# Optimization experiments

Hardware: AMD Instinct MI355X
Metric: run time of the kernel (lower is better)

## Reference

```python
import jax, jax.numpy as jnp
import numpy as np

B, S, HID, H, D, F = 8, 256, 1024, 16, 64, 64
BASE_LR = 0.1
MAX_STEPS = 4
EPS = 1e-5


def _ln(x, g, b):
    mu = jnp.mean(x, axis=-1, keepdims=True)
    var = jnp.var(x, axis=-1, keepdims=True)
    return (x - mu) * jax.lax.rsqrt(var + EPS) * g + b


def setup_inputs() -> dict:
    key = jax.random.key(0)
    ks = jax.random.split(key, 10)
    n = lambda i, shape, s=0.02: jax.random.normal(ks[i], shape, jnp.float32) * s
    return {
        "x": jax.random.normal(ks[0], (B, S, HID), jnp.float32),
        "wq": n(1, (HID, HID)),
        "wk": n(2, (HID, HID)),
        "wv": n(3, (HID, HID)),
        "fw_w1": n(4, (H, D, F), 0.05),
        "fw_b1": jnp.zeros((H, F), jnp.float32),
        "fw_w2": n(5, (H, F, D), 0.05),
        "fw_b2": jnp.zeros((H, D), jnp.float32),
        "fw_ln_g": jnp.ones((H, D), jnp.float32),
        "fw_ln_b": jnp.zeros((H, D), jnp.float32),
        "loss_w": n(6, (D, D)),
        "loss_b": jnp.zeros((D,), jnp.float32),
        "ttt_g": jnp.ones((H, D), jnp.float32),
        "ttt_b": jnp.zeros((H, D), jnp.float32),
        "wo": n(7, (HID, HID)),
        "wg": n(8, (HID, HID)),
        "pn_g": jnp.ones((HID,), jnp.float32),
        "pn_b": jnp.zeros((HID,), jnp.float32),
    }


def _fw_apply(p, kx):
    # per-head fast-weight MLP: kx (B,H,D) -> (B,H,D)
    w1, b1, w2, b2, lg, lb = p
    h = jax.nn.gelu(jnp.einsum('bhd,hdf->bhf', kx, w1) + b1)
    o = jnp.einsum('bhf,hfd->bhd', h, w2) + b2
    return _ln(o, lg, lb)


def _forward(x, wq, wk, wv, fw_w1, fw_b1, fw_w2, fw_b2, fw_ln_g, fw_ln_b,
             loss_w, loss_b, ttt_g, ttt_b, wo, wg, pn_g, pn_b):
    # projections (torch Linear with W stored as (in,out) here: y = x @ W)
    q = (x @ wq).reshape(B, S, H, D)
    k = (x @ wk).reshape(B, S, H, D)
    v = (x @ wv).reshape(B, S, H, D)
    # scan over tokens: xs shaped (S, B, H, D)
    qs = jnp.swapaxes(q, 0, 1)
    ks_ = jnp.swapaxes(k, 0, 1)
    vs = jnp.swapaxes(v, 0, 1)

    def token_step(p, qkv):
        q_t, k_t, v_t = qkv  # (B,H,D) each
        target = v_t - k_t

        def loss_fn(pp):
            z = _fw_apply(pp, k_t)
            pred = jnp.einsum('bhd,de->bhe', z, loss_w) + loss_b
            return jnp.mean((pred - target) ** 2)

        for _ in range(MAX_STEPS):
            g = jax.grad(loss_fn)(p)
            p = jax.tree.map(lambda a, gg: a - BASE_LR * gg, p, g)
        z = _fw_apply(p, k_t)
        z = _ln(z, ttt_g, ttt_b)  # per-head post-TTT LayerNorm
        return p, q_t + z

    p0 = (fw_w1, fw_b1, fw_w2, fw_b2, fw_ln_g, fw_ln_b)
    _, outs = jax.lax.scan(token_step, p0, (qs, ks_, vs))
    out = jnp.swapaxes(outs, 0, 1).reshape(B, S, HID)
    gated = jax.nn.gelu(x @ wg) * _ln(out, pn_g, pn_b)
    return gated @ wo


def reference(x, wq, wk, wv, fw_w1, fw_b1, fw_w2, fw_b2, fw_ln_g, fw_ln_b,
              loss_w, loss_b, ttt_g, ttt_b, wo, wg, pn_g, pn_b):
    return _forward(x, wq, wk, wv, fw_w1, fw_b1, fw_w2, fw_b2, fw_ln_g, fw_ln_b,
                    loss_w, loss_b, ttt_g, ttt_b, wo, wg, pn_g, pn_b)
```

## Files before the change

### kernel.cpp

```cpp
#include <hip/hip_runtime.h>

#define Bv 8
#define Sv 256
#define Hv 16
#define Dv 64
#define LR 0.1f
#define SCALE (2.0f / 8192.0f)

using bf16x8 = __attribute__((ext_vector_type(8))) short;
using bf16x4 = __attribute__((ext_vector_type(4))) short;
using f32x4  = __attribute__((ext_vector_type(4))) float;
using u32x4  = __attribute__((ext_vector_type(4))) unsigned;
#define MFMA16(A, B, C) __builtin_amdgcn_mfma_f32_16x16x32_bf16(A, B, C, 0, 0, 0)

constexpr int U_W1T = 0;
constexpr int U_W2T = 8704;
constexpr int U_W2R = 17408;
constexpr int U_G   = 26112;
constexpr int U_LwR = 34816;
constexpr int U_K   = 43520;
constexpr int U_H   = 45696;
constexpr int U_Z   = 47872;
constexpr int U_TG  = 50048;
constexpr int U_DO  = 52224;
constexpr int U_KT  = 54400;
constexpr int U_HT  = 55424;
constexpr int U_DOT = 56448;
constexpr int U_DAT = 57472;
constexpr int F_BASE = 29248;
constexpr int F_O   = F_BASE;
constexpr int F_XH  = F_BASE + 544;
constexpr int F_GD  = F_XH + 544;
constexpr int F_TGL = F_GD + 544;
constexpr int F_B1  = F_TGL + 544;
constexpr int F_B2  = F_B1 + 64;
constexpr int F_LG  = F_B2 + 64;
constexpr int F_LB  = F_LG + 64;
constexpr int F_C1  = F_LB + 64;
constexpr int F_TGm = F_C1 + 64;
constexpr int F_TBm = F_TGm + 64;
constexpr int F_RSTD = F_TBm + 64;
constexpr int U_KG  = (F_RSTD + 8) * 2;
constexpr int U_HT2 = U_KG + 256;
constexpr int LDS_BYTES = (U_HT2 + 1024) * 2;

__device__ __forceinline__ short bf_rn(float v) {
    unsigned u = __float_as_uint(v);
    unsigned r = u + 0x7fffu + ((u >> 16) & 1u);
    return (short)(r >> 16);
}
__device__ __forceinline__ void cvt1(float v, short &hi, short &lo) {
    hi = bf_rn(v);
    float hf = __uint_as_float(((unsigned)(unsigned short)hi) << 16);
    lo = bf_rn(v - hf);
}
__device__ __forceinline__ float bf2f(short u) {
    return __uint_as_float(((unsigned)(unsigned short)u) << 16);
}
__device__ __forceinline__ unsigned cvtpk(float a, float b) {
    unsigned r;
    asm("v_cvt_pk_bf16_f32 %0, %1, %2" : "=v"(r) : "v"(a), "v"(b));
    return r;
}
__device__ __forceinline__ void cvt2(float a, float b, unsigned &hw,
                                     unsigned &lw) {
    hw = cvtpk(a, b);
    float ra = a - __uint_as_float(hw << 16);
    float rb = b - __uint_as_float(hw & 0xffff0000u);
    lw = cvtpk(ra, rb);
}
template <int CTRL>
__device__ __forceinline__ float dpp_add(float v) {
    int s = __builtin_amdgcn_update_dpp(0, __float_as_int(v), CTRL, 0xF, 0xF,
                                        true);
    return v + __int_as_float(s);
}
__device__ __forceinline__ float red32(float v) {
    v = dpp_add<0xB1>(v);
    v = dpp_add<0x4E>(v);
    v = dpp_add<0x124>(v);
    v = dpp_add<0x128>(v);
    v += __shfl_xor(v, 16);
    return v;
}
__device__ __forceinline__ float fast_tanh(float u) {
    u = fminf(fmaxf(u, -10.f), 10.f);
    float e = __expf(2.0f * u);
    return (e - 1.0f) / (e + 1.0f);
}
__device__ __forceinline__ void gelu_both(float x, float &g, float &dg) {
    const float C0 = 0.7978845608028654f, A0 = 0.044715f;
    float x2 = x * x;
    float u = C0 * x * (1.0f + A0 * x2);
    float t = fast_tanh(u);
    g = 0.5f * x * (1.0f + t);
    float du = C0 * (1.0f + 3.0f * A0 * x2);
    dg = 0.5f * (1.0f + t) + 0.5f * x * (1.0f - t * t) * du;
}
__device__ __forceinline__ float gelu_f(float x) {
    const float C0 = 0.7978845608028654f, A0 = 0.044715f;
    float u = C0 * x * (1.0f + A0 * x * x);
    return 0.5f * x * (1.0f + fast_tanh(u));
}

__device__ __forceinline__ f32x4 mm64(const unsigned short *Ap,
                                      const unsigned short *Bp,
                                      int w, int c, int q) {
    const unsigned short *ar = Ap + c * 136 + 8 * q;
    const unsigned short *br = Bp + (16 * w + c) * 136 + 8 * q;
    bf16x8 ah0 = *(const bf16x8 *)(ar);
    bf16x8 al0 = *(const bf16x8 *)(ar + 64);
    bf16x8 bh0 = *(const bf16x8 *)(br);
    bf16x8 bl0 = *(const bf16x8 *)(br + 64);
    bf16x8 ah1 = *(const bf16x8 *)(ar + 32);
    bf16x8 al1 = *(const bf16x8 *)(ar + 96);
    bf16x8 bh1 = *(const bf16x8 *)(br + 32);
    bf16x8 bl1 = *(const bf16x8 *)(br + 96);
    f32x4 x0 = {0.f, 0.f, 0.f, 0.f}, x1 = {0.f, 0.f, 0.f, 0.f};
    x0 = MFMA16(ah0, bh0, x0); x1 = MFMA16(ah1, bh1, x1);
    x0 = MFMA16(al0, bh0, x0); x1 = MFMA16(al1, bh1, x1);
    x0 = MFMA16(ah0, bl0, x0); x1 = MFMA16(ah1, bl1, x1);
    return x0 + x1;
}

__device__ __forceinline__ void updW3(const bf16x8 *a4, bf16x8 b,
                                      float (&m)[16], unsigned short *WT,
                                      int w, int c, int q) {
    f32x4 g[4];
#pragma unroll
    for (int mt = 0; mt < 4; ++mt) {
        f32x4 z = {0.f, 0.f, 0.f, 0.f};
        g[mt] = MFMA16(a4[mt], b, z);
    }
    unsigned short *p0 = &WT[(16 * w + c) * 136 + 4 * q];
#pragma unroll
    for (int mt = 0; mt < 4; ++mt) {
        m[mt * 4 + 0] -= LR * g[mt][0];
        m[mt * 4 + 1] -= LR * g[mt][1];
        m[mt * 4 + 2] -= LR * g[mt][2];
        m[mt * 4 + 3] -= LR * g[mt][3];
        unsigned nh0, nl0, nh1, nl1;
        cvt2(m[mt * 4 + 0], m[mt * 4 + 1], nh0, nl0);
        cvt2(m[mt * 4 + 2], m[mt * 4 + 3], nh1, nl1);
        uint2 nh, nl;
        nh.x = nh0; nh.y = nh1;
        nl.x = nl0; nl.y = nl1;
        *(uint2 *)(p0 + 16 * mt) = nh;
        *(uint2 *)(p0 + 16 * mt + 64) = nl;
    }
}

__global__ __launch_bounds__(256) void ttt_scan(
    const float *__restrict__ q_g, const float *__restrict__ k_g,
    const float *__restrict__ v_g, float *__restrict__ out_g,
    const float *__restrict__ fw_w1, const float *__restrict__ fw_b1,
    const float *__restrict__ fw_w2, const float *__restrict__ fw_b2,
    const float *__restrict__ fw_lng, const float *__restrict__ fw_lnb,
    const float *__restrict__ loss_w, const float *__restrict__ loss_bv,
    const float *__restrict__ ttt_gv, const float *__restrict__ ttt_bv) {
    extern __shared__ char smem[];
    unsigned short *us = (unsigned short *)smem;
    float *fs = (float *)smem;

    unsigned short *W1T = us + U_W1T, *W2T = us + U_W2T, *W2R = us + U_W2R;
    unsigned short *Gp = us + U_G, *LwR = us + U_LwR;
    unsigned short *Kp = us + U_K, *Hp = us + U_H, *Zp = us + U_Z;
    unsigned short *TGp = us + U_TG, *DOp = us + U_DO;
    unsigned short *KT = us + U_KT, *HT0 = us + U_HT;
    unsigned short *DOT = us + U_DOT;
    unsigned short *KgT = us + U_KG, *HT1 = us + U_HT2;
    float *o_s = fs + F_O, *xh_s = fs + F_XH;
    float *b2_s = fs + F_B2, *lg_s = fs + F_LG;
    float *lb_s = fs + F_LB, *c1_s = fs + F_C1;
    float *tG_s = fs + F_TGm, *tB_s = fs + F_TBm, *rstd_s = fs + F_RSTD;

    const int h = blockIdx.x, tid = threadIdx.x;
    const int w = tid >> 6, lane = tid & 63, c = lane & 15, q = lane >> 4;
    const int bb = tid >> 5, j0 = (tid & 31) * 2;

    for (int i = tid; i < 4096; i += 256) {
        int r = i >> 6, cc = i & 63;
        short hi, lo;
        cvt1(fw_w1[h * 4096 + i], hi, lo);
        W1T[cc * 136 + r] = (unsigned short)hi;
        W1T[cc * 136 + 64 + r] = (unsigned short)lo;
        cvt1(fw_w2[h * 4096 + i], hi, lo);
        W2T[cc * 136 + r] = (unsigned short)hi;
        W2T[cc * 136 + 64 + r] = (unsigned short)lo;
        W2R[r * 136 + cc] = (unsigned short)hi;
        W2R[r * 136 + 64 + cc] = (unsigned short)lo;
        cvt1(loss_w[i], hi, lo);
        LwR[r * 136 + cc] = (unsigned short)hi;
        LwR[r * 136 + 64 + cc] = (unsigned short)lo;
    }
    for (int i = tid; i < 5 * 8 * 128; i += 256) {
        int a = i / 128, u = i % 128;
        int arr = a >> 3, row = 8 + (a & 7);
        unsigned short *base = (arr == 0) ? Kp : (arr == 1) ? Hp
                              : (arr == 2) ? Zp : (arr == 3) ? TGp : DOp;
        base[row * 136 + u] = 0;
    }
    float w1m[16], w2m[16], w2rm[16];
#pragma unroll
    for (int mt = 0; mt < 4; ++mt) {
#pragma unroll
        for (int r = 0; r < 4; ++r) {
            int el = 16 * mt + 4 * q + r;
            int row = 16 * w + c;
            w1m[mt * 4 + r] = fw_w1[h * 4096 + el * 64 + row];
            w2m[mt * 4 + r] = fw_w2[h * 4096 + el * 64 + row];
            w2rm[mt * 4 + r] = fw_w2[h * 4096 + row * 64 + el];
        }
    }
    __syncthreads();
#pragma unroll 1
    for (int mt = 0; mt < 4; ++mt) {
        f32x4 g = mm64(LwR + 16 * 136 * mt, LwR, w, c, q);
#pragma unroll
        for (int r = 0; r < 4; ++r) {
            short hi, lo;
            cvt1(g[r], hi, lo);
            int dr = 16 * mt + 4 * q + r, dc = 16 * w + c;
            Gp[dr * 136 + dc] = (unsigned short)hi;
            Gp[dr * 136 + 64 + dc] = (unsigned short)lo;
        }
    }
    if (tid < 64) {
        b2_s[tid] = fw_b2[h * 64 + tid];
        lg_s[tid] = fw_lng[h * 64 + tid];
        lb_s[tid] = fw_lnb[h * 64 + tid];
        tG_s[tid] = ttt_gv[h * 64 + tid];
        tB_s[tid] = ttt_bv[h * 64 + tid];
        float c1 = 0.f;
        for (int e = 0; e < 64; ++e) c1 += loss_bv[e] * loss_w[tid * 64 + e];
        c1_s[tid] = c1;
    }

    float2 pk, pv, pq, q_cur;
    {
        int idx = ((bb * Sv + 0) * Hv + h) * Dv + j0;
        float2 k0 = *(const float2 *)&k_g[idx];
        float2 v0 = *(const float2 *)&v_g[idx];
        q_cur = *(const float2 *)&q_g[idx];
        unsigned khw, klw;
        cvt2(k0.x, k0.y, khw, klw);
        *(unsigned *)&Kp[bb * 136 + j0] = khw;
        *(unsigned *)&Kp[bb * 136 + 64 + j0] = klw;
        KT[j0 * 16 + bb] = (unsigned short)khw;
        KT[j0 * 16 + 8 + bb] = (unsigned short)klw;
        KT[(j0 + 1) * 16 + bb] = (unsigned short)(khw >> 16);
        KT[(j0 + 1) * 16 + 8 + bb] = (unsigned short)(klw >> 16);
        unsigned thw, tlw;
        cvt2(v0.x - k0.x, v0.y - k0.y, thw, tlw);
        *(unsigned *)&TGp[bb * 136 + j0] = thw;
        *(unsigned *)&TGp[bb * 136 + 64 + j0] = tlw;
    }
    float b1_r = (q < 2) ? fw_b1[h * 64 + 16 * w + c] : 0.f;
    __syncthreads();
    float c1_r = c1_s[16 * w + c];
    f32x4 gd_r = {0.f, 0.f, 0.f, 0.f};
    f32x4 tgl_r = {0.f, 0.f, 0.f, 0.f};

#pragma unroll 1
    for (int t = 0; t < Sv; ++t) {
        if (t + 1 < Sv) {
            int idx2 = ((bb * Sv + t + 1) * Hv + h) * Dv + j0;
            pk = *(const float2 *)&k_g[idx2];
            pv = *(const float2 *)&v_g[idx2];
            pq = *(const float2 *)&q_g[idx2];
        }

        f32x4 acc1 = mm64(Kp, W1T, w, c, q);
        {
            f32x4 a2 = mm64(TGp, LwR, w, c, q);
            if (q < 2) {
#pragma unroll
                for (int r = 0; r < 4; ++r) tgl_r[r] = a2[r] - c1_r;
            }
        }
        if (w == 0) {
            f32x4 kg = mm64(Kp, Kp, 0, c, q);
            if (q < 2) {
#pragma unroll
                for (int r = 0; r < 4; ++r) {
                    short hi, lo;
                    cvt1(-LR * kg[r], hi, lo);
                    KgT[c * 16 + 4 * q + r] = (unsigned short)hi;
                    KgT[c * 16 + 8 + 4 * q + r] = (unsigned short)lo;
                }
            }
        }
        if (q < 2) {
            int col = 16 * w + c;
            float gv[4];
#pragma unroll
            for (int r = 0; r < 4; ++r) {
                float g, dg;
                gelu_both(acc1[r] + b1_r, g, dg);
                gv[r] = g;
                gd_r[r] = dg;
            }
            unsigned h01, l01, h23, l23;
            cvt2(gv[0], gv[1], h01, l01);
            cvt2(gv[2], gv[3], h23, l23);
            Hp[(4 * q + 0) * 136 + col] = (unsigned short)h01;
            Hp[(4 * q + 1) * 136 + col] = (unsigned short)(h01 >> 16);
            Hp[(4 * q + 2) * 136 + col] = (unsigned short)h23;
            Hp[(4 * q + 3) * 136 + col] = (unsigned short)(h23 >> 16);
            Hp[(4 * q + 0) * 136 + 64 + col] = (unsigned short)l01;
            Hp[(4 * q + 1) * 136 + 64 + col] = (unsigned short)(l01 >> 16);
            Hp[(4 * q + 2) * 136 + 64 + col] = (unsigned short)l23;
            Hp[(4 * q + 3) * 136 + 64 + col] = (unsigned short)(l23 >> 16);
            uint2 hh, hl;
            hh.x = h01; hh.y = h23;
            hl.x = l01; hl.y = l23;
            *(uint2 *)&HT0[col * 16 + 4 * q] = hh;
            *(uint2 *)&HT0[col * 16 + 8 + 4 * q] = hl;
        }
        __syncthreads();

#pragma unroll 1
        for (int step = 0; step < 4; ++step) {
            const unsigned short *HTr = (step & 1) ? HT1 : HT0;
            unsigned short *HTw = (step & 1) ? HT0 : HT1;
            f32x4 acc = mm64(Hp, W2T, w, c, q);
            if (q < 2) {
                float bias = b2_s[16 * w + c];
#pragma unroll
                for (int r = 0; r < 4; ++r)
                    o_s[(4 * q + r) * 68 + 16 * w + c] = acc[r] + bias;
            }
            __syncthreads();
            float xh0_r, xh1_r;
            {
                float2 xv = *(const float2 *)&o_s[bb * 68 + j0];
                float s = red32(xv.x + xv.y);
                float s2 = red32(xv.x * xv.x + xv.y * xv.y);
                float mu = s * (1.f / 64.f);
                float var = s2 * (1.f / 64.f) - mu * mu;
                float rs = rsqrtf(var + 1e-5f);
                float xh0 = (xv.x - mu) * rs, xh1 = (xv.y - mu) * rs;
                float2 xw; xw.x = xh0; xw.y = xh1;
                *(float2 *)&xh_s[bb * 68 + j0] = xw;
                float z0 = xh0 * lg_s[j0] + lb_s[j0];
                float z1 = xh1 * lg_s[j0 + 1] + lb_s[j0 + 1];
                unsigned zh, zl;
                cvt2(z0, z1, zh, zl);
                *(unsigned *)&Zp[bb * 136 + j0] = zh;
                *(unsigned *)&Zp[bb * 136 + 64 + j0] = zl;
                if ((tid & 31) == 0) rstd_s[bb] = rs;
                xh0_r = xh0; xh1_r = xh1;
            }
            __syncthreads();
            acc = mm64(Zp, Gp, w, c, q);
            if (q < 2) {
                int col = 16 * w + c;
#pragma unroll
                for (int r = 0; r < 4; ++r)
                    o_s[(4 * q + r) * 68 + col] = (acc[r] - tgl_r[r]) * SCALE;
            }
            __syncthreads();
            {
                float2 dzv = *(const float2 *)&o_s[bb * 68 + j0];
                float dxh0 = dzv.x * lg_s[j0], dxh1 = dzv.y * lg_s[j0 + 1];
                float S1 = red32(dxh0 + dxh1) * (1.f / 64.f);
                float S2 = red32(dxh0 * xh0_r + dxh1 * xh1_r) * (1.f / 64.f);
                float rs = rstd_s[bb];
                float do0 = rs * (dxh0 - S1 - xh0_r * S2);
                float do1 = rs * (dxh1 - S1 - xh1_r * S2);
                unsigned dh, dl;
                cvt2(do0, do1, dh, dl);
                *(unsigned *)&DOp[bb * 136 + j0] = dh;
                *(unsigned *)&DOp[bb * 136 + 64 + j0] = dl;
                DOT[j0 * 16 + bb] = (unsigned short)dh;
                DOT[j0 * 16 + 8 + bb] = (unsigned short)dl;
                DOT[(j0 + 1) * 16 + bb] = (unsigned short)(dh >> 16);
                DOT[(j0 + 1) * 16 + 8 + bb] = (unsigned short)(dl >> 16);
            }
            __syncthreads();
            bf16x8 zf8;
#pragma unroll
            for (int j = 0; j < 8; ++j) zf8[j] = 0;
            bf16x8 aK[4], aH[4], aD[4];
#pragma unroll
            for (int mt = 0; mt < 4; ++mt) {
                aK[mt] = *(const bf16x8 *)&KT[(16 * mt + c) * 16 + (q & 1) * 8];
                aH[mt] = *(const bf16x8 *)&HTr[(16 * mt + c) * 16 + (q & 1) * 8];
                aD[mt] = *(const bf16x8 *)&DOT[(16 * mt + c) * 16 + (q & 1) * 8];
            }
            bf16x8 bDO = zf8, bHT = zf8;
            if (q < 2) {
                bDO = *(const bf16x8 *)&DOT[(16 * w + c) * 16];
                bHT = *(const bf16x8 *)&HTr[(16 * w + c) * 16];
            } else if (q == 2) {
                bDO = *(const bf16x8 *)&DOT[(16 * w + c) * 16 + 8];
                bHT = *(const bf16x8 *)&HTr[(16 * w + c) * 16 + 8];
            }
            bf16x8 aKg = *(const bf16x8 *)&KgT[c * 16 + (q & 1) * 8];
            acc = mm64(DOp, W2R, w, c, q);
            {
                float b1sum = 0.f;
                uint2 th; th.x = 0u; th.y = 0u;
                uint2 tl; tl.x = 0u; tl.y = 0u;
                if (q < 2) {
                    float da0 = acc[0] * gd_r[0];
                    float da1 = acc[1] * gd_r[1];
                    float da2 = acc[2] * gd_r[2];
                    float da3 = acc[3] * gd_r[3];
                    b1sum = da0 + da1 + da2 + da3;
                    unsigned h01, l01, h23, l23;
                    cvt2(da0, da1, h01, l01);
                    cvt2(da2, da3, h23, l23);
                    th.x = h01; th.y = h23;
                    tl.x = l01; tl.y = l23;
                }
                b1sum += __shfl_xor(b1sum, 16);
                unsigned hx0 = (unsigned)__shfl((int)th.x, c);
                unsigned hy0 = (unsigned)__shfl((int)th.y, c);
                unsigned hx1 = (unsigned)__shfl((int)th.x, c + 16);
                unsigned hy1 = (unsigned)__shfl((int)th.y, c + 16);
                unsigned lx0 = (unsigned)__shfl((int)tl.x, c);
                unsigned ly0 = (unsigned)__shfl((int)tl.y, c);
                unsigned lx1 = (unsigned)__shfl((int)tl.x, c + 16);
                unsigned ly1 = (unsigned)__shfl((int)tl.y, c + 16);
                u32x4 Bw = {0u, 0u, 0u, 0u};
                if (q < 2) {
                    Bw[0] = hx0; Bw[1] = hy0; Bw[2] = hx1; Bw[3] = hy1;
                } else if (q == 2) {
                    Bw[0] = lx0; Bw[1] = ly0; Bw[2] = lx1; Bw[3] = ly1;
                }
                bf16x8 bDA = __builtin_bit_cast(bf16x8, Bw);
                updW3(aK, bDA, w1m, W1T, w, c, q);
                updW3(aH, bDO, w2m, W2T, w, c, q);
                updW3(aD, bHT, w2rm, W2R, w, c, q);
                if (w == 2) {
                    bf16x8 oh_ = *(const bf16x8 *)&DOT[lane * 16];
                    bf16x8 ol_ = *(const bf16x8 *)&DOT[lane * 16 + 8];
                    float db2 = 0.f;
#pragma unroll
                    for (int j = 0; j < 8; ++j)
                        db2 += bf2f(oh_[j]) + bf2f(ol_[j]);
                    b2_s[lane] -= LR * db2;
                } else if (w == 3) {
                    float dlb = 0.f, dlg = 0.f;
#pragma unroll
                    for (int b = 0; b < 8; ++b) {
                        float dzv = o_s[b * 68 + lane];
                        dlb += dzv;
                        dlg += dzv * xh_s[b * 68 + lane];
                    }
                    lb_s[lane] -= LR * dlb;
                    lg_s[lane] -= LR * dlg;
                }
                acc1 = MFMA16(aKg, bDA, acc1);
                b1_r -= LR * b1sum;
                if (q < 2) {
                    int col = 16 * w + c;
                    if (step < 3) {
                        float gv[4];
#pragma unroll
                        for (int r = 0; r < 4; ++r) {
                            float g, dg;
                            gelu_both(acc1[r] + b1_r, g, dg);
                            gv[r] = g;
                            gd_r[r] = dg;
                        }
                        unsigned h01, l01, h23, l23;
                        cvt2(gv[0], gv[1], h01, l01);
                        cvt2(gv[2], gv[3], h23, l23);
                        Hp[(4 * q + 0) * 136 + col] = (unsigned short)h01;
                        Hp[(4 * q + 1) * 136 + col] = (unsigned short)(h01 >> 16);
                        Hp[(4 * q + 2) * 136 + col] = (unsigned short)h23;
                        Hp[(4 * q + 3) * 136 + col] = (unsigned short)(h23 >> 16);
                        Hp[(4 * q + 0) * 136 + 64 + col] = (unsigned short)l01;
                        Hp[(4 * q + 1) * 136 + 64 + col] = (unsigned short)(l01 >> 16);
                        Hp[(4 * q + 2) * 136 + 64 + col] = (unsigned short)l23;
                        Hp[(4 * q + 3) * 136 + 64 + col] = (unsigned short)(l23 >> 16);
                        uint2 hh, hl;
                        hh.x = h01; hh.y = h23;
                        hl.x = l01; hl.y = l23;
                        *(uint2 *)&HTw[col * 16 + 4 * q] = hh;
                        *(uint2 *)&HTw[col * 16 + 8 + 4 * q] = hl;
                    } else {
                        float gv[4];
#pragma unroll
                        for (int r = 0; r < 4; ++r)
                            gv[r] = gelu_f(acc1[r] + b1_r);
                        unsigned h01, l01, h23, l23;
                        cvt2(gv[0], gv[1], h01, l01);
                        cvt2(gv[2], gv[3], h23, l23);
                        Hp[(4 * q + 0) * 136 + col] = (unsigned short)h01;
                        Hp[(4 * q + 1) * 136 + col] = (unsigned short)(h01 >> 16);
                        Hp[(4 * q + 2) * 136 + col] = (unsigned short)h23;
                        Hp[(4 * q + 3) * 136 + col] = (unsigned short)(h23 >> 16);
                        Hp[(4 * q + 0) * 136 + 64 + col] = (unsigned short)l01;
                        Hp[(4 * q + 1) * 136 + 64 + col] = (unsigned short)(l01 >> 16);
                        Hp[(4 * q + 2) * 136 + 64 + col] = (unsigned short)l23;
                        Hp[(4 * q + 3) * 136 + 64 + col] = (unsigned short)(l23 >> 16);
                    }
                }
            }
            __syncthreads();
        }

        f32x4 acc = mm64(Hp, W2T, w, c, q);
        if (q < 2) {
            float bias = b2_s[16 * w + c];
#pragma unroll
            for (int r = 0; r < 4; ++r)
                o_s[(4 * q + r) * 68 + 16 * w + c] = acc[r] + bias;
        }
        if (t + 1 < Sv) {
            unsigned khw, klw;
            cvt2(pk.x, pk.y, khw, klw);
            *(unsigned *)&Kp[bb * 136 + j0] = khw;
            *(unsigned *)&Kp[bb * 136 + 64 + j0] = klw;
            KT[j0 * 16 + bb] = (unsigned short)khw;
            KT[j0 * 16 + 8 + bb] = (unsigned short)klw;
            KT[(j0 + 1) * 16 + bb] = (unsigned short)(khw >> 16);
            KT[(j0 + 1) * 16 + 8 + bb] = (unsigned short)(klw >> 16);
            unsigned thw, tlw;
            cvt2(pv.x - pk.x, pv.y - pk.y, thw, tlw);
            *(unsigned *)&TGp[bb * 136 + j0] = thw;
            *(unsigned *)&TGp[bb * 136 + 64 + j0] = tlw;
        }
        __syncthreads();
        {
            float2 xv = *(const float2 *)&o_s[bb * 68 + j0];
            float s = red32(xv.x + xv.y);
            float s2 = red32(xv.x * xv.x + xv.y * xv.y);
            float mu = s * (1.f / 64.f);
            float var = s2 * (1.f / 64.f) - mu * mu;
            float rs = rsqrtf(var + 1e-5f);
            float z0 = (xv.x - mu) * rs * lg_s[j0] + lb_s[j0];
            float z1 = (xv.y - mu) * rs * lg_s[j0 + 1] + lb_s[j0 + 1];
            float sb = red32(z0 + z1);
            float s2b = red32(z0 * z0 + z1 * z1);
            float mu2 = sb * (1.f / 64.f);
            float var2 = s2b * (1.f / 64.f) - mu2 * mu2;
            float rs2 = rsqrtf(var2 + 1e-5f);
            float z20 = (z0 - mu2) * rs2 * tG_s[j0] + tB_s[j0];
            float z21 = (z1 - mu2) * rs2 * tG_s[j0 + 1] + tB_s[j0 + 1];
            int idx = ((bb * Sv + t) * Hv + h) * Dv + j0;
            float2 ov;
            ov.x = q_cur.x + z20;
            ov.y = q_cur.y + z21;
            *(float2 *)&out_g[idx] = ov;
            q_cur = pq;
        }
    }
}

__global__ __launch_bounds__(256) void gemm_f32(
    const float *__restrict__ A, const float *__restrict__ B,
    float *__restrict__ C, const float *__restrict__ gate_ln,
    int M, int N, int K, int mode) {
    __shared__ float As[16][68];
    __shared__ float Bs[16][64];
    const int tid = threadIdx.x;
    const int tx = tid & 15, ty = tid >> 4;
    const int bm = blockIdx.y * 64, bn = blockIdx.x * 64;

    float acc[4][4] = {};
    for (int k0 = 0; k0 < K; k0 += 16) {
        {
            int r = tid >> 2, kk = (tid & 3) * 4;
            float4 av = *(const float4 *)(A + (long)(bm + r) * K + k0 + kk);
            As[kk + 0][r] = av.x;
            As[kk + 1][r] = av.y;
            As[kk + 2][r] = av.z;
            As[kk + 3][r] = av.w;
            int rr = tid >> 4, cc = (tid & 15) * 4;
            float4 bv = *(const float4 *)(B + (long)(k0 + rr) * N + bn + cc);
            *(float4 *)&Bs[rr][cc] = bv;
        }
        __syncthreads();
#pragma unroll
        for (int kk = 0; kk < 16; ++kk) {
            float4 a4 = *(float4 *)&As[kk][ty * 4];
            float4 b4 = *(float4 *)&Bs[kk][tx * 4];
            float a[4] = {a4.x, a4.y, a4.z, a4.w};
            float b[4] = {b4.x, b4.y, b4.z, b4.w};
#pragma unroll
            for (int i = 0; i < 4; ++i)
#pragma unroll
                for (int j = 0; j < 4; ++j) acc[i][j] += a[i] * b[j];
        }
        __syncthreads();
    }
#pragma unroll
    for (int i = 0; i < 4; ++i) {
        int row = bm + ty * 4 + i;
        float4 out;
        float v[4];
#pragma unroll
        for (int j = 0; j < 4; ++j) {
            float val = acc[i][j];
            if (mode == 1) {
                int col = bn + tx * 4 + j;
                val = gelu_f(val) * gate_ln[(long)row * N + col];
            }
            v[j] = val;
        }
        out.x = v[0]; out.y = v[1]; out.z = v[2]; out.w = v[3];
        *(float4 *)(C + (long)row * N + bn + tx * 4) = out;
    }
}

__global__ __launch_bounds__(256) void row_ln(const float *__restrict__ in,
                                              float *__restrict__ out,
                                              const float *__restrict__ g,
                                              const float *__restrict__ b) {
    __shared__ float sred[4], s2red[4];
    const int row = blockIdx.x;
    const int tid = threadIdx.x;
    const float *x = in + (long)row * 1024;
    float4 v = *(const float4 *)(x + tid * 4);
    float s = v.x + v.y + v.z + v.w;
    float s2 = v.x * v.x + v.y * v.y + v.z * v.z + v.w * v.w;
#pragma unroll
    for (int m = 1; m <= 32; m <<= 1) {
        s += __shfl_xor(s, m);
        s2 += __shfl_xor(s2, m);
    }
    if ((tid & 63) == 0) {
        sred[tid >> 6] = s;
        s2red[tid >> 6] = s2;
    }
    __syncthreads();
    float S = sred[0] + sred[1] + sred[2] + sred[3];
    float S2 = s2red[0] + s2red[1] + s2red[2] + s2red[3];
    float mu = S * (1.f / 1024.f);
    float var = S2 * (1.f / 1024.f) - mu * mu;
    float rs = rsqrtf(var + 1e-5f);
    float o[4] = {v.x, v.y, v.z, v.w};
    float4 ov;
    float r[4];
#pragma unroll
    for (int i = 0; i < 4; ++i) {
        int col = tid * 4 + i;
        r[i] = (o[i] - mu) * rs * g[col] + b[col];
    }
    ov.x = r[0]; ov.y = r[1]; ov.z = r[2]; ov.w = r[3];
    *(float4 *)(out + (long)row * 1024 + tid * 4) = ov;
}

extern "C" void kernel_launch(void *const *d_in, const int *in_sizes, int n_in,
                              void *d_out, int out_size, void *d_ws,
                              size_t ws_size, hipStream_t stream) {
    const float *x = (const float *)d_in[0];
    const float *wq = (const float *)d_in[1];
    const float *wk = (const float *)d_in[2];
    const float *wv = (const float *)d_in[3];
    const float *fw_w1 = (const float *)d_in[4];
    const float *fw_b1 = (const float *)d_in[5];
    const float *fw_w2 = (const float *)d_in[6];
    const float *fw_b2 = (const float *)d_in[7];
    const float *fw_lng = (const float *)d_in[8];
    const float *fw_lnb = (const float *)d_in[9];
    const float *loss_w = (const float *)d_in[10];
    const float *loss_b = (const float *)d_in[11];
    const float *ttt_g = (const float *)d_in[12];
    const float *ttt_b = (const float *)d_in[13];
    const float *wo = (const float *)d_in[14];
    const float *wg = (const float *)d_in[15];
    const float *pn_g = (const float *)d_in[16];
    const float *pn_b = (const float *)d_in[17];

    const long MAT = 2048L * 1024L;
    float *q_ws = (float *)d_ws;
    float *k_ws = q_ws + MAT;
    float *v_ws = k_ws + MAT;
    float *out_ws = v_ws + MAT;
    float *ln_ws = k_ws;
    float *gated_ws = v_ws;

    dim3 gg(1024 / 64, 2048 / 64), bt(256);
    hipLaunchKernelGGL(gemm_f32, gg, bt, 0, stream, x, wq, q_ws,
                       (const float *)nullptr, 2048, 1024, 1024, 0);
    hipLaunchKernelGGL(gemm_f32, gg, bt, 0, stream, x, wk, k_ws,
                       (const float *)nullptr, 2048, 1024, 1024, 0);
    hipLaunchKernelGGL(gemm_f32, gg, bt, 0, stream, x, wv, v_ws,
                       (const float *)nullptr, 2048, 1024, 1024, 0);

    (void)hipFuncSetAttribute((const void *)ttt_scan,
                              hipFuncAttributeMaxDynamicSharedMemorySize,
                              LDS_BYTES);
    hipLaunchKernelGGL(ttt_scan, dim3(16), dim3(256), LDS_BYTES, stream,
                       q_ws, k_ws, v_ws, out_ws, fw_w1, fw_b1, fw_w2, fw_b2,
                       fw_lng, fw_lnb, loss_w, loss_b, ttt_g, ttt_b);

    hipLaunchKernelGGL(row_ln, dim3(2048), dim3(256), 0, stream, out_ws, ln_ws,
                       pn_g, pn_b);
    hipLaunchKernelGGL(gemm_f32, gg, bt, 0, stream, x, wg, gated_ws, ln_ws,
                       2048, 1024, 1024, 1);
    hipLaunchKernelGGL(gemm_f32, gg, bt, 0, stream, gated_ws, wo,
                       (float *)d_out, (const float *)nullptr, 2048, 1024,
                       1024, 0);
}
```

Baseline: 3.920 ms.

## Replace FP32 SIMT GEMMs with split-bf16 MFMA GEMMs

Measured after the change: 3.760 ms. 4.1% less time.

```diff
diff --git a/kernel.cpp b/kernel.cpp
--- a/kernel.cpp
+++ b/kernel.cpp
@@ -551,59 +551,83 @@
     }
 }
 
-__global__ __launch_bounds__(256) void gemm_f32(
+__global__ __launch_bounds__(256) void gemm_bf16(
     const float *__restrict__ A, const float *__restrict__ B,
     float *__restrict__ C, const float *__restrict__ gate_ln,
     int M, int N, int K, int mode) {
-    __shared__ float As[16][68];
-    __shared__ float Bs[16][64];
+    __shared__ unsigned short As[64 * 136];
+    __shared__ unsigned short Bs[64 * 136];
     const int tid = threadIdx.x;
-    const int tx = tid & 15, ty = tid >> 4;
+    const int w = tid >> 6, lane = tid & 63, c = lane & 15, q = lane >> 4;
     const int bm = blockIdx.y * 64, bn = blockIdx.x * 64;
 
-    float acc[4][4] = {};
-    for (int k0 = 0; k0 < K; k0 += 16) {
+    f32x4 acc[4] = {{0.f, 0.f, 0.f, 0.f}, {0.f, 0.f, 0.f, 0.f},
+                    {0.f, 0.f, 0.f, 0.f}, {0.f, 0.f, 0.f, 0.f}};
+    const int srow = tid >> 2, sseg = (tid & 3) * 16;
+
+    for (int k0 = 0; k0 < K; k0 += 64) {
         {
-            int r = tid >> 2, kk = (tid & 3) * 4;
-            float4 av = *(const float4 *)(A + (long)(bm + r) * K + k0 + kk);
-            As[kk + 0][r] = av.x;
-            As[kk + 1][r] = av.y;
-            As[kk + 2][r] = av.z;
-            As[kk + 3][r] = av.w;
-            int rr = tid >> 4, cc = (tid & 15) * 4;
-            float4 bv = *(const float4 *)(B + (long)(k0 + rr) * N + bn + cc);
-            *(float4 *)&Bs[rr][cc] = bv;
+            const float *src = A + (long)(bm + srow) * K + k0 + sseg;
+#pragma unroll
+            for (int j = 0; j < 16; j += 2) {
+                float2 v = *(const float2 *)(src + j);
+                unsigned hw, lw;
+                cvt2(v.x, v.y, hw, lw);
+                *(unsigned *)&As[srow * 136 + sseg + j] = hw;
+                *(unsigned *)&As[srow * 136 + 64 + sseg + j] = lw;
+            }
+        }
+        {
+            const float *bsrc = B + (long)(k0 + srow) * N + bn + sseg;
+#pragma unroll
+            for (int j = 0; j < 16; j += 4) {
+                float4 v = *(const float4 *)(bsrc + j);
+                short hi, lo;
+                cvt1(v.x, hi, lo);
+                Bs[(sseg + j + 0) * 136 + srow] = (unsigned short)hi;
+                Bs[(sseg + j + 0) * 136 + 64 + srow] = (unsigned short)lo;
+                cvt1(v.y, hi, lo);
+                Bs[(sseg + j + 1) * 136 + srow] = (unsigned short)hi;
+                Bs[(sseg + j + 1) * 136 + 64 + srow] = (unsigned short)lo;
+                cvt1(v.z, hi, lo);
+                Bs[(sseg + j + 2) * 136 + srow] = (unsigned short)hi;
+                Bs[(sseg + j + 2) * 136 + 64 + srow] = (unsigned short)lo;
+                cvt1(v.w, hi, lo);
+                Bs[(sseg + j + 3) * 136 + srow] = (unsigned short)hi;
+                Bs[(sseg + j + 3) * 136 + 64 + srow] = (unsigned short)lo;
+            }
         }
         __syncthreads();
 #pragma unroll
-        for (int kk = 0; kk < 16; ++kk) {
-            float4 a4 = *(float4 *)&As[kk][ty * 4];
-            float4 b4 = *(float4 *)&Bs[kk][tx * 4];
-            float a[4] = {a4.x, a4.y, a4.z, a4.w};
-            float b[4] = {b4.x, b4.y, b4.z, b4.w};
-#pragma unroll
-            for (int i = 0; i < 4; ++i)
-#pragma unroll
-                for (int j = 0; j < 4; ++j) acc[i][j] += a[i] * b[j];
+        for (int kc = 0; kc < 2; ++kc) {
+            const unsigned short *br =
+                &Bs[(16 * w + c) * 136 + kc * 32 + 8 * q];
+            bf16x8 bh = *(const bf16x8 *)(br);
+            bf16x8 bl = *(const bf16x8 *)(br + 64);
+#pragma unroll
+            for (int mt = 0; mt < 4; ++mt) {
+                const unsigned short *ar =
+                    &As[(16 * mt + c) * 136 + kc * 32 + 8 * q];
+                bf16x8 ah = *(const bf16x8 *)(ar);
+                bf16x8 al = *(const bf16x8 *)(ar + 64);
+                acc[mt] = MFMA16(ah, bh, acc[mt]);
+                acc[mt] = MFMA16(al, bh, acc[mt]);
+                acc[mt] = MFMA16(ah, bl, acc[mt]);
+            }
         }
         __syncthreads();
     }
 #pragma unroll
-    for (int i = 0; i < 4; ++i) {
-        int row = bm + ty * 4 + i;
-        float4 out;
-        float v[4];
-#pragma unroll
-        for (int j = 0; j < 4; ++j) {
-            float val = acc[i][j];
-            if (mode == 1) {
-                int col = bn + tx * 4 + j;
+    for (int mt = 0; mt < 4; ++mt) {
+#pragma unroll
+        for (int r = 0; r < 4; ++r) {
+            int row = bm + 16 * mt + 4 * q + r;
+            int col = bn + 16 * w + c;
+            float val = acc[mt][r];
+            if (mode == 1)
                 val = gelu_f(val) * gate_ln[(long)row * N + col];
-            }
-            v[j] = val;
-        }
-        out.x = v[0]; out.y = v[1]; out.z = v[2]; out.w = v[3];
-        *(float4 *)(C + (long)row * N + bn + tx * 4) = out;
+            C[(long)row * N + col] = val;
+        }
     }
 }
 
@@ -676,11 +700,11 @@
     float *gated_ws = v_ws;
 
     dim3 gg(1024 / 64, 2048 / 64), bt(256);
-    hipLaunchKernelGGL(gemm_f32, gg, bt, 0, stream, x, wq, q_ws,
+    hipLaunchKernelGGL(gemm_bf16, gg, bt, 0, stream, x, wq, q_ws,
                        (const float *)nullptr, 2048, 1024, 1024, 0);
-    hipLaunchKernelGGL(gemm_f32, gg, bt, 0, stream, x, wk, k_ws,
+    hipLaunchKernelGGL(gemm_bf16, gg, bt, 0, stream, x, wk, k_ws,
                        (const float *)nullptr, 2048, 1024, 1024, 0);
-    hipLaunchKernelGGL(gemm_f32, gg, bt, 0, stream, x, wv, v_ws,
+    hipLaunchKernelGGL(gemm_bf16, gg, bt, 0, stream, x, wv, v_ws,
                        (const float *)nullptr, 2048, 1024, 1024, 0);
 
     (void)hipFuncSetAttribute((const void *)ttt_scan,
@@ -692,9 +716,9 @@
 
     hipLaunchKernelGGL(row_ln, dim3(2048), dim3(256), 0, stream, out_ws, ln_ws,
                        pn_g, pn_b);
-    hipLaunchKernelGGL(gemm_f32, gg, bt, 0, stream, x, wg, gated_ws, ln_ws,
+    hipLaunchKernelGGL(gemm_bf16, gg, bt, 0, stream, x, wg, gated_ws, ln_ws,
                        2048, 1024, 1024, 1);
-    hipLaunchKernelGGL(gemm_f32, gg, bt, 0, stream, gated_ws, wo,
+    hipLaunchKernelGGL(gemm_bf16, gg, bt, 0, stream, gated_ws, wo,
                        (float *)d_out, (const float *)nullptr, 2048, 1024,
                        1024, 0);
 }
```
